# Kernel tuning notes

Measured on AMD Instinct MI355X. Metric: run time of the kernel, lower is better.

Reference implementation:

```python
import jax, jax.numpy as jnp
import numpy as np

N_NODES = 8192
IN_DIM = 128
HIDDEN = 128
N_EDGES = 262144


def gcn_layer(x, W, b, src, dst, n):
    # GCNConv: h = D^{-1/2}(A+I)D^{-1/2} (x @ W) + b, with added self-loops
    h = x @ W  # [n, out]
    loop = jnp.arange(n, dtype=src.dtype)
    s = jnp.concatenate([src, loop])
    d = jnp.concatenate([dst, loop])
    deg = jax.ops.segment_sum(jnp.ones_like(s, dtype=h.dtype), d, num_segments=n)
    dinv = jax.lax.rsqrt(deg)  # deg >= 1 due to self-loops
    norm = dinv[s] * dinv[d]  # [E+n]
    msg = h[s] * norm[:, None]
    out = jax.ops.segment_sum(msg, d, num_segments=n)
    return out + b


def setup_inputs() -> dict:
    key = jax.random.key(0)
    ks = jax.random.split(key, 10)
    g = 1.0 / np.sqrt(HIDDEN)
    inp = {
        "x": jax.random.normal(ks[0], (N_NODES, IN_DIM), dtype=jnp.float32),
        "edge_index": jax.random.randint(ks[1], (2, N_EDGES), 0, N_NODES, dtype=jnp.int32),
        "W1": jax.random.normal(ks[2], (IN_DIM, HIDDEN), dtype=jnp.float32) * (1.0 / np.sqrt(IN_DIM)),
        "b1": jnp.zeros((HIDDEN,), dtype=jnp.float32),
        "W2": jax.random.normal(ks[3], (HIDDEN, HIDDEN), dtype=jnp.float32) * g,
        "b2": jnp.zeros((HIDDEN,), dtype=jnp.float32),
        "W_out": jax.random.normal(ks[4], (HIDDEN, HIDDEN), dtype=jnp.float32) * g,
        "b_out": jnp.zeros((HIDDEN,), dtype=jnp.float32),
        "W_edge": jax.random.normal(ks[5], (2 * HIDDEN,), dtype=jnp.float32) * (1.0 / np.sqrt(2 * HIDDEN)),
        "b_edge": jnp.zeros((), dtype=jnp.float32),
    }
    return inp


def reference(x, edge_index, W1, b1, W2, b2, W_out, b_out, W_edge, b_edge):
    src, dst = edge_index[0], edge_index[1]
    n = x.shape[0]
    h = jax.nn.relu(gcn_layer(x, W1, b1, src, dst, n))
    h = jax.nn.relu(gcn_layer(h, W2, b2, src, dst, n))
    h = h @ W_out + b_out  # [n, hidden]
    # edge_proj(cat(x_i, x_j)) decomposes: logits[i,j] = h_i.w_i + h_j.w_j + b
    w_i, w_j = W_edge[:HIDDEN], W_edge[HIDDEN:]
    a = h @ w_i  # [n]
    c = h @ w_j  # [n]
    edge_logits = a[:, None] + c[None, :] + b_edge  # [n, n]
    return edge_logits
```

## Files before the change

### kernel.cpp

```cpp
#include <hip/hip_runtime.h>

#define NN 8192
#define NE 262144
#define DIM 128
#define BCAP 128

typedef float f32x4 __attribute__((ext_vector_type(4)));
typedef float f32x2 __attribute__((ext_vector_type(2)));

__device__ __forceinline__ float4 f4fma(float s, float4 w, float4 acc) {
    acc.x = fmaf(s, w.x, acc.x);
    acc.y = fmaf(s, w.y, acc.y);
    acc.z = fmaf(s, w.z, acc.z);
    acc.w = fmaf(s, w.w, acc.w);
    return acc;
}
__device__ __forceinline__ float f4dot(float4 a, float4 b) {
    return fmaf(a.x, b.x, fmaf(a.y, b.y, fmaf(a.z, b.z, a.w * b.w)));
}

__global__ __launch_bounds__(256) void zero_kernel(int* __restrict__ cnt) {
    cnt[blockIdx.x * 256 + threadIdx.x] = 0;
}

__global__ __launch_bounds__(256) void fused_pre(const float* __restrict__ X,
                                                 const float* __restrict__ W,
                                                 float* __restrict__ G,
                                                 const int* __restrict__ src,
                                                 const int* __restrict__ dst,
                                                 int* __restrict__ cnt,
                                                 int* __restrict__ bucket,
                                                 const float* __restrict__ Wout,
                                                 const float* __restrict__ bout,
                                                 const float* __restrict__ we,
                                                 const float* __restrict__ bedge,
                                                 float* __restrict__ u,
                                                 float* __restrict__ v,
                                                 float* __restrict__ beta) {
    __shared__ float4 Wl[128 * 32];
    __shared__ float4 Xl[32 * 32];
    int tid = threadIdx.x;
    int bid = blockIdx.x;

    if (bid < 256) {
        int rbase = bid * 32;
        const float4* W4 = (const float4*)W;
#pragma unroll
        for (int i = 0; i < 16; ++i) Wl[i * 256 + tid] = W4[i * 256 + tid];
        const float4* X4 = (const float4*)(X + rbase * DIM);
#pragma unroll
        for (int i = 0; i < 4; ++i) Xl[i * 256 + tid] = X4[i * 256 + tid];
        __syncthreads();

        int tx = tid & 31;
        int ty = tid >> 5;
        float4 acc[4];
#pragma unroll
        for (int i = 0; i < 4; ++i) acc[i] = make_float4(0.f, 0.f, 0.f, 0.f);

        for (int k4 = 0; k4 < 32; ++k4) {
            float4 w0 = Wl[(k4 * 4 + 0) * 32 + tx];
            float4 w1 = Wl[(k4 * 4 + 1) * 32 + tx];
            float4 w2 = Wl[(k4 * 4 + 2) * 32 + tx];
            float4 w3 = Wl[(k4 * 4 + 3) * 32 + tx];
#pragma unroll
            for (int i = 0; i < 4; ++i) {
                float4 xv = Xl[(ty * 4 + i) * 32 + k4];
                acc[i] = f4fma(xv.x, w0, acc[i]);
                acc[i] = f4fma(xv.y, w1, acc[i]);
                acc[i] = f4fma(xv.z, w2, acc[i]);
                acc[i] = f4fma(xv.w, w3, acc[i]);
            }
        }
        float4* G4 = (float4*)G;
#pragma unroll
        for (int i = 0; i < 4; ++i) {
            int r = rbase + ty * 4 + i;
            G4[r * 32 + tx] = acc[i];
        }
        return;
    }
    if (bid < 1280) {
        int e = (bid - 256) * 256 + tid;
        int d = dst[e];
        int p = atomicAdd(&cnt[d], 1);
        if (p < BCAP) bucket[(d << 7) + p] = src[e];
        return;
    }
    float* red = (float*)Xl;
    int k = tid;
    if (k < DIM) {
        const float4* W4o = (const float4*)(Wout + (k << 7));
        const float4* we4 = (const float4*)we;
        float su = 0.f, sv = 0.f;
#pragma unroll
        for (int j = 0; j < 32; ++j) {
            float4 w = W4o[j];
            su += f4dot(w, we4[j]);
            sv += f4dot(w, we4[32 + j]);
        }
        u[k] = su;
        v[k] = sv;
    }
    red[k] = (k < DIM) ? bout[k] * we[k] : 0.f;
    __syncthreads();
    for (int off = 128; off >= 1; off >>= 1) {
        if (k < off) red[k] += red[k + off];
        __syncthreads();
    }
    float b0 = red[0];
    __syncthreads();
    red[k] = (k < DIM) ? bout[k] * we[DIM + k] : 0.f;
    __syncthreads();
    for (int off = 128; off >= 1; off >>= 1) {
        if (k < off) red[k] += red[k + off];
        __syncthreads();
    }
    if (k == 0) {
        beta[0] = b0 + bedge[0];
        beta[1] = red[0];
    }
}

__global__ __launch_bounds__(256) void gather_scale(const float* __restrict__ G1,
                                                    const int* __restrict__ cnt,
                                                    const int* __restrict__ bucket,
                                                    const float* __restrict__ b1,
                                                    float* __restrict__ S2) {
    int node = blockIdx.x * 4 + (threadIdx.x >> 6);
    int lane = threadIdx.x & 63;
    const float2* G12 = (const float2*)G1;

    int degree = cnt[node];
    float dv = rsqrtf((float)(degree + 1));
    int deg = min(degree, BCAP);
    int i0 = bucket[(node << 7) + lane];
    int i1 = bucket[(node << 7) + 64 + lane];

    float2 selfv = G12[node * 64 + lane];
    float ax = selfv.x * dv, ay = selfv.y * dv;
    float px[8], py[8];
#pragma unroll
    for (int k = 0; k < 8; ++k) { px[k] = 0.f; py[k] = 0.f; }

    int d8 = deg & ~7;
    for (int e = 0; e < d8; e += 8) {
        int s[8];
#pragma unroll
        for (int k = 0; k < 8; ++k) s[k] = __shfl((e + k) >= 64 ? i1 : i0, (e + k) & 63);
#pragma unroll
        for (int k = 0; k < 8; ++k) {
            int ck = cnt[s[k]];
            float2 t = G12[s[k] * 64 + lane];
            float w = rsqrtf((float)(ck + 1));
            px[k] = fmaf(t.x, w, px[k]);
            py[k] = fmaf(t.y, w, py[k]);
        }
    }
    for (int e = d8; e < deg; ++e) {
        int s = __shfl(e >= 64 ? i1 : i0, e & 63);
        int ck = cnt[s];
        float2 t = G12[s * 64 + lane];
        float w = rsqrtf((float)(ck + 1));
        ax = fmaf(t.x, w, ax);
        ay = fmaf(t.y, w, ay);
    }
    float yx = ax + ((px[0] + px[1]) + (px[2] + px[3])) + ((px[4] + px[5]) + (px[6] + px[7]));
    float yy = ay + ((py[0] + py[1]) + (py[2] + py[3])) + ((py[4] + py[5]) + (py[6] + py[7]));

    const float2* B2 = (const float2*)b1;
    float2 bb = B2[lane];
    float2 o;
    o.x = fmaxf(fmaf(yx, dv, bb.x), 0.f) * dv;
    o.y = fmaxf(fmaf(yy, dv, bb.y), 0.f) * dv;
    ((float2*)S2)[node * 64 + lane] = o;
}

__global__ __launch_bounds__(256) void gemm_mid(const float* __restrict__ X,
                                                const float* __restrict__ W,
                                                float* __restrict__ G) {
    __shared__ float4 Wl[128 * 32];
    __shared__ float4 Xl[32 * 32];
    int tid = threadIdx.x;
    int rbase = blockIdx.x * 32;

    const float4* W4 = (const float4*)W;
#pragma unroll
    for (int i = 0; i < 16; ++i) Wl[i * 256 + tid] = W4[i * 256 + tid];
    const float4* X4 = (const float4*)(X + rbase * DIM);
#pragma unroll
    for (int i = 0; i < 4; ++i) Xl[i * 256 + tid] = X4[i * 256 + tid];
    __syncthreads();

    int tx = tid & 31;
    int ty = tid >> 5;
    float4 acc[4];
#pragma unroll
    for (int i = 0; i < 4; ++i) acc[i] = make_float4(0.f, 0.f, 0.f, 0.f);

    for (int k4 = 0; k4 < 32; ++k4) {
        float4 w0 = Wl[(k4 * 4 + 0) * 32 + tx];
        float4 w1 = Wl[(k4 * 4 + 1) * 32 + tx];
        float4 w2 = Wl[(k4 * 4 + 2) * 32 + tx];
        float4 w3 = Wl[(k4 * 4 + 3) * 32 + tx];
#pragma unroll
        for (int i = 0; i < 4; ++i) {
            float4 xv = Xl[(ty * 4 + i) * 32 + k4];
            acc[i] = f4fma(xv.x, w0, acc[i]);
            acc[i] = f4fma(xv.y, w1, acc[i]);
            acc[i] = f4fma(xv.z, w2, acc[i]);
            acc[i] = f4fma(xv.w, w3, acc[i]);
        }
    }

    float4* G4 = (float4*)G;
#pragma unroll
    for (int i = 0; i < 4; ++i) {
        int r = rbase + ty * 4 + i;
        G4[r * 32 + tx] = acc[i];
    }
}

__global__ __launch_bounds__(256) void agg_head(const float* __restrict__ G2,
                                                const int* __restrict__ cnt,
                                                const int* __restrict__ bucket,
                                                const float* __restrict__ b2,
                                                const float* __restrict__ u,
                                                const float* __restrict__ v,
                                                const float* __restrict__ beta,
                                                float* __restrict__ a,
                                                float* __restrict__ c) {
    int node = blockIdx.x * 4 + (threadIdx.x >> 6);
    int lane = threadIdx.x & 63;
    const float2* G22 = (const float2*)G2;

    int degree = cnt[node];
    float dv = rsqrtf((float)(degree + 1));
    int deg = min(degree, BCAP);
    int i0 = bucket[(node << 7) + lane];
    int i1 = bucket[(node << 7) + 64 + lane];

    float2 selfv = G22[node * 64 + lane];
    float ax = selfv.x, ay = selfv.y;
    float px[8], py[8];
#pragma unroll
    for (int k = 0; k < 8; ++k) { px[k] = 0.f; py[k] = 0.f; }

    int d8 = deg & ~7;
    for (int e = 0; e < d8; e += 8) {
        int s[8];
#pragma unroll
        for (int k = 0; k < 8; ++k) s[k] = __shfl((e + k) >= 64 ? i1 : i0, (e + k) & 63);
#pragma unroll
        for (int k = 0; k < 8; ++k) {
            float2 t = G22[s[k] * 64 + lane];
            px[k] += t.x;
            py[k] += t.y;
        }
    }
    for (int e = d8; e < deg; ++e) {
        int s = __shfl(e >= 64 ? i1 : i0, e & 63);
        float2 t = G22[s * 64 + lane];
        ax += t.x;
        ay += t.y;
    }
    float yx = ax + ((px[0] + px[1]) + (px[2] + px[3])) + ((px[4] + px[5]) + (px[6] + px[7]));
    float yy = ay + ((py[0] + py[1]) + (py[2] + py[3])) + ((py[4] + py[5]) + (py[6] + py[7]));

    const float2* B2 = (const float2*)b2;
    float2 bb = B2[lane];
    float h0 = fmaxf(fmaf(yx, dv, bb.x), 0.f);
    float h1 = fmaxf(fmaf(yy, dv, bb.y), 0.f);

    float2 uu = ((const float2*)u)[lane];
    float2 vv = ((const float2*)v)[lane];
    float pa = h0 * uu.x + h1 * uu.y;
    float pc = h0 * vv.x + h1 * vv.y;
#pragma unroll
    for (int off = 32; off >= 1; off >>= 1) {
        pa += __shfl_xor(pa, off);
        pc += __shfl_xor(pc, off);
    }
    if (lane == 0) {
        a[node] = pa + beta[0];
        c[node] = pc + beta[1];
    }
}

__global__ __launch_bounds__(256) void out_kernel(const float* __restrict__ a,
                                                  const float* __restrict__ c,
                                                  f32x4* __restrict__ out) {
    const f32x4* c4 = (const f32x4*)c;
    size_t base = (size_t)blockIdx.x * 1024 + threadIdx.x;
#pragma unroll
    for (int q = 0; q < 4; ++q) {
        size_t idx = base + q * 256;
        int i = (int)(idx >> 11);
        int j4 = (int)(idx & 2047);
        f32x4 r = c4[j4] + a[i];
        out[idx] = r;
    }
}

extern "C" void kernel_launch(void* const* d_in, const int* in_sizes, int n_in,
                              void* d_out, int out_size, void* d_ws, size_t ws_size,
                              hipStream_t stream) {
    const float* x    = (const float*)d_in[0];
    const int*   ei   = (const int*)d_in[1];
    const float* W1   = (const float*)d_in[2];
    const float* b1   = (const float*)d_in[3];
    const float* W2   = (const float*)d_in[4];
    const float* b2   = (const float*)d_in[5];
    const float* Wout = (const float*)d_in[6];
    const float* bout = (const float*)d_in[7];
    const float* We   = (const float*)d_in[8];
    const float* bedge= (const float*)d_in[9];
    const int* src = ei;
    const int* dst = ei + NE;

    int* cnt     = (int*)d_ws;
    int* bucket  = cnt + NN;
    float* u     = (float*)(bucket + NN * BCAP);
    float* v     = u + DIM;
    float* beta  = v + DIM;
    float* g1    = beta + 16;
    float* s2    = g1 + NN * DIM;
    float* g2    = s2 + NN * DIM;
    float* av    = g2 + NN * DIM;
    float* cv    = av + NN;

    float* out = (float*)d_out;

    zero_kernel<<<32, 256, 0, stream>>>(cnt);
    fused_pre<<<1281, 256, 0, stream>>>(x, W1, g1, src, dst, cnt, bucket,
                                        Wout, bout, We, bedge, u, v, beta);
    gather_scale<<<NN / 4, 256, 0, stream>>>(g1, cnt, bucket, b1, s2);
    gemm_mid<<<NN / 32, 256, 0, stream>>>(s2, W2, g2);
    agg_head<<<NN / 4, 256, 0, stream>>>(g2, cnt, bucket, b2, u, v, beta, av, cv);
    out_kernel<<<(NN * NN / 4) / 1024, 256, 0, stream>>>(av, cv, (f32x4*)out);
}
```

Before: 109.1 us.

## Split neighbor gathers across half-waves with 16-byte loads and precomputed weights

The two aggregation kernels now give each half of a 64-lane wave a different neighbor, and each lane loads a float4 instead of a float2. The two halves' partial sums are combined with a cross-half shuffle. In gather_scale, each neighbor's degree weight is computed once per lane up front and broadcast by shuffle, instead of being reloaded inside the loop. Padded tail iterations use zero weights instead of a scalar remainder loop, and bucket reads become nontemporal loads. The aim is more memory-level parallelism and fewer load instructions for the random row gathers, at the cost of extra shuffles and some wasted padded loads.

Result: faster. 101.9 us (-6.6%).

```diff
diff --git a/kernel.cpp b/kernel.cpp
--- a/kernel.cpp
+++ b/kernel.cpp
@@ -17,6 +17,13 @@
 }
 __device__ __forceinline__ float f4dot(float4 a, float4 b) {
     return fmaf(a.x, b.x, fmaf(a.y, b.y, fmaf(a.z, b.z, a.w * b.w)));
+}
+__device__ __forceinline__ f32x4 vfma(f32x4 t, float w, f32x4 acc) {
+    acc.x = fmaf(t.x, w, acc.x);
+    acc.y = fmaf(t.y, w, acc.y);
+    acc.z = fmaf(t.z, w, acc.z);
+    acc.w = fmaf(t.w, w, acc.w);
+    return acc;
 }
 
 __global__ __launch_bounds__(256) void zero_kernel(int* __restrict__ cnt) {
@@ -129,51 +136,81 @@
                                                     float* __restrict__ S2) {
     int node = blockIdx.x * 4 + (threadIdx.x >> 6);
     int lane = threadIdx.x & 63;
-    const float2* G12 = (const float2*)G1;
+    int half = lane >> 5;
+    int fl = lane & 31;
+    const f32x4* G14 = (const f32x4*)G1;
 
     int degree = cnt[node];
     float dv = rsqrtf((float)(degree + 1));
     int deg = min(degree, BCAP);
-    int i0 = bucket[(node << 7) + lane];
-    int i1 = bucket[(node << 7) + 64 + lane];
-
-    float2 selfv = G12[node * 64 + lane];
-    float ax = selfv.x * dv, ay = selfv.y * dv;
-    float px[8], py[8];
-#pragma unroll
-    for (int k = 0; k < 8; ++k) { px[k] = 0.f; py[k] = 0.f; }
-
-    int d8 = deg & ~7;
-    for (int e = 0; e < d8; e += 8) {
-        int s[8];
-#pragma unroll
-        for (int k = 0; k < 8; ++k) s[k] = __shfl((e + k) >= 64 ? i1 : i0, (e + k) & 63);
-#pragma unroll
-        for (int k = 0; k < 8; ++k) {
-            int ck = cnt[s[k]];
-            float2 t = G12[s[k] * 64 + lane];
-            float w = rsqrtf((float)(ck + 1));
-            px[k] = fmaf(t.x, w, px[k]);
-            py[k] = fmaf(t.y, w, py[k]);
-        }
-    }
-    for (int e = d8; e < deg; ++e) {
-        int s = __shfl(e >= 64 ? i1 : i0, e & 63);
-        int ck = cnt[s];
-        float2 t = G12[s * 64 + lane];
-        float w = rsqrtf((float)(ck + 1));
-        ax = fmaf(t.x, w, ax);
-        ay = fmaf(t.y, w, ay);
-    }
-    float yx = ax + ((px[0] + px[1]) + (px[2] + px[3])) + ((px[4] + px[5]) + (px[6] + px[7]));
-    float yy = ay + ((py[0] + py[1]) + (py[2] + py[3])) + ((py[4] + py[5]) + (py[6] + py[7]));
-
-    const float2* B2 = (const float2*)b1;
-    float2 bb = B2[lane];
-    float2 o;
-    o.x = fmaxf(fmaf(yx, dv, bb.x), 0.f) * dv;
-    o.y = fmaxf(fmaf(yy, dv, bb.y), 0.f) * dv;
-    ((float2*)S2)[node * 64 + lane] = o;
+    int a0 = __builtin_nontemporal_load(bucket + (node << 7) + lane);
+    int a1 = __builtin_nontemporal_load(bucket + (node << 7) + 64 + lane);
+    int i0s = (lane < deg) ? a0 : 0;
+    int i1s = (64 + lane < deg) ? a1 : 0;
+    float w0 = (lane < deg) ? rsqrtf((float)(cnt[i0s] + 1)) : 0.f;
+    float w1 = (64 + lane < deg) ? rsqrtf((float)(cnt[i1s] + 1)) : 0.f;
+
+    f32x4 zero4 = {0.f, 0.f, 0.f, 0.f};
+    f32x4 p0 = zero4, p1 = zero4, p2 = zero4, p3 = zero4;
+    f32x4 self4 = G14[node * 32 + fl];
+    f32x4 acc = zero4;
+    if (half == 0) {
+        acc.x = self4.x * dv; acc.y = self4.y * dv;
+        acc.z = self4.z * dv; acc.w = self4.w * dv;
+    }
+
+    int L1 = min(deg, 64);
+    int E1 = (L1 + 7) & ~7;
+    for (int e = 0; e < E1; e += 8) {
+        int q = e + half;
+        int s0 = __shfl(i0s, q);     float q0w = __shfl(w0, q);
+        int s1 = __shfl(i0s, q + 2); float q1w = __shfl(w0, q + 2);
+        int s2 = __shfl(i0s, q + 4); float q2w = __shfl(w0, q + 4);
+        int s3 = __shfl(i0s, q + 6); float q3w = __shfl(w0, q + 6);
+        f32x4 t0 = G14[s0 * 32 + fl];
+        f32x4 t1 = G14[s1 * 32 + fl];
+        f32x4 t2 = G14[s2 * 32 + fl];
+        f32x4 t3 = G14[s3 * 32 + fl];
+        p0 = vfma(t0, q0w, p0);
+        p1 = vfma(t1, q1w, p1);
+        p2 = vfma(t2, q2w, p2);
+        p3 = vfma(t3, q3w, p3);
+    }
+    if (deg > 64) {
+        int L2 = deg - 64;
+        int E2 = (L2 + 7) & ~7;
+        for (int e = 0; e < E2; e += 8) {
+            int q = e + half;
+            int s0 = __shfl(i1s, q);     float q0w = __shfl(w1, q);
+            int s1 = __shfl(i1s, q + 2); float q1w = __shfl(w1, q + 2);
+            int s2 = __shfl(i1s, q + 4); float q2w = __shfl(w1, q + 4);
+            int s3 = __shfl(i1s, q + 6); float q3w = __shfl(w1, q + 6);
+            f32x4 t0 = G14[s0 * 32 + fl];
+            f32x4 t1 = G14[s1 * 32 + fl];
+            f32x4 t2 = G14[s2 * 32 + fl];
+            f32x4 t3 = G14[s3 * 32 + fl];
+            p0 = vfma(t0, q0w, p0);
+            p1 = vfma(t1, q1w, p1);
+            p2 = vfma(t2, q2w, p2);
+            p3 = vfma(t3, q3w, p3);
+        }
+    }
+
+    f32x4 sum = ((p0 + p1) + (p2 + p3)) + acc;
+    f32x4 oth;
+    oth.x = __shfl_xor(sum.x, 32);
+    oth.y = __shfl_xor(sum.y, 32);
+    oth.z = __shfl_xor(sum.z, 32);
+    oth.w = __shfl_xor(sum.w, 32);
+    sum += oth;
+
+    f32x4 bb = ((const f32x4*)b1)[fl];
+    f32x4 o;
+    o.x = fmaxf(fmaf(sum.x, dv, bb.x), 0.f) * dv;
+    o.y = fmaxf(fmaf(sum.y, dv, bb.y), 0.f) * dv;
+    o.z = fmaxf(fmaf(sum.z, dv, bb.z), 0.f) * dv;
+    o.w = fmaxf(fmaf(sum.w, dv, bb.w), 0.f) * dv;
+    if (half == 0) ((f32x4*)S2)[node * 32 + fl] = o;
 }
 
 __global__ __launch_bounds__(256) void gemm_mid(const float* __restrict__ X,
@@ -232,52 +269,88 @@
                                                 float* __restrict__ c) {
     int node = blockIdx.x * 4 + (threadIdx.x >> 6);
     int lane = threadIdx.x & 63;
-    const float2* G22 = (const float2*)G2;
+    int half = lane >> 5;
+    int fl = lane & 31;
+    const f32x4* G24 = (const f32x4*)G2;
 
     int degree = cnt[node];
     float dv = rsqrtf((float)(degree + 1));
     int deg = min(degree, BCAP);
-    int i0 = bucket[(node << 7) + lane];
-    int i1 = bucket[(node << 7) + 64 + lane];
-
-    float2 selfv = G22[node * 64 + lane];
-    float ax = selfv.x, ay = selfv.y;
-    float px[8], py[8];
-#pragma unroll
-    for (int k = 0; k < 8; ++k) { px[k] = 0.f; py[k] = 0.f; }
-
-    int d8 = deg & ~7;
-    for (int e = 0; e < d8; e += 8) {
-        int s[8];
-#pragma unroll
-        for (int k = 0; k < 8; ++k) s[k] = __shfl((e + k) >= 64 ? i1 : i0, (e + k) & 63);
-#pragma unroll
-        for (int k = 0; k < 8; ++k) {
-            float2 t = G22[s[k] * 64 + lane];
-            px[k] += t.x;
-            py[k] += t.y;
-        }
-    }
-    for (int e = d8; e < deg; ++e) {
-        int s = __shfl(e >= 64 ? i1 : i0, e & 63);
-        float2 t = G22[s * 64 + lane];
-        ax += t.x;
-        ay += t.y;
-    }
-    float yx = ax + ((px[0] + px[1]) + (px[2] + px[3])) + ((px[4] + px[5]) + (px[6] + px[7]));
-    float yy = ay + ((py[0] + py[1]) + (py[2] + py[3])) + ((py[4] + py[5]) + (py[6] + py[7]));
-
-    const float2* B2 = (const float2*)b2;
-    float2 bb = B2[lane];
-    float h0 = fmaxf(fmaf(yx, dv, bb.x), 0.f);
-    float h1 = fmaxf(fmaf(yy, dv, bb.y), 0.f);
-
-    float2 uu = ((const float2*)u)[lane];
-    float2 vv = ((const float2*)v)[lane];
-    float pa = h0 * uu.x + h1 * uu.y;
-    float pc = h0 * vv.x + h1 * vv.y;
-#pragma unroll
-    for (int off = 32; off >= 1; off >>= 1) {
+    int a0 = __builtin_nontemporal_load(bucket + (node << 7) + lane);
+    int a1 = __builtin_nontemporal_load(bucket + (node << 7) + 64 + lane);
+    int i0s = (lane < deg) ? a0 : 0;
+    int i1s = (64 + lane < deg) ? a1 : 0;
+
+    f32x4 zero4 = {0.f, 0.f, 0.f, 0.f};
+    f32x4 p0 = zero4, p1 = zero4, p2 = zero4, p3 = zero4;
+    f32x4 acc = (half == 0) ? G24[node * 32 + fl] : zero4;
+
+    int L1 = min(deg, 64);
+    int E1 = (L1 + 7) & ~7;
+    for (int e = 0; e < E1; e += 8) {
+        int q = e + half;
+        int s0 = __shfl(i0s, q);
+        int s1 = __shfl(i0s, q + 2);
+        int s2 = __shfl(i0s, q + 4);
+        int s3 = __shfl(i0s, q + 6);
+        float q0w = (q < L1) ? 1.f : 0.f;
+        float q1w = (q + 2 < L1) ? 1.f : 0.f;
+        float q2w = (q + 4 < L1) ? 1.f : 0.f;
+        float q3w = (q + 6 < L1) ? 1.f : 0.f;
+        f32x4 t0 = G24[s0 * 32 + fl];
+        f32x4 t1 = G24[s1 * 32 + fl];
+        f32x4 t2 = G24[s2 * 32 + fl];
+        f32x4 t3 = G24[s3 * 32 + fl];
+        p0 = vfma(t0, q0w, p0);
+        p1 = vfma(t1, q1w, p1);
+        p2 = vfma(t2, q2w, p2);
+        p3 = vfma(t3, q3w, p3);
+    }
+    if (deg > 64) {
+        int L2 = deg - 64;
+        int E2 = (L2 + 7) & ~7;
+        for (int e = 0; e < E2; e += 8) {
+            int q = e + half;
+            int s0 = __shfl(i1s, q);
+            int s1 = __shfl(i1s, q + 2);
+            int s2 = __shfl(i1s, q + 4);
+            int s3 = __shfl(i1s, q + 6);
+            float q0w = (q < L2) ? 1.f : 0.f;
+            float q1w = (q + 2 < L2) ? 1.f : 0.f;
+            float q2w = (q + 4 < L2) ? 1.f : 0.f;
+            float q3w = (q + 6 < L2) ? 1.f : 0.f;
+            f32x4 t0 = G24[s0 * 32 + fl];
+            f32x4 t1 = G24[s1 * 32 + fl];
+            f32x4 t2 = G24[s2 * 32 + fl];
+            f32x4 t3 = G24[s3 * 32 + fl];
+            p0 = vfma(t0, q0w, p0);
+            p1 = vfma(t1, q1w, p1);
+            p2 = vfma(t2, q2w, p2);
+            p3 = vfma(t3, q3w, p3);
+        }
+    }
+
+    f32x4 sum = ((p0 + p1) + (p2 + p3)) + acc;
+    f32x4 oth;
+    oth.x = __shfl_xor(sum.x, 32);
+    oth.y = __shfl_xor(sum.y, 32);
+    oth.z = __shfl_xor(sum.z, 32);
+    oth.w = __shfl_xor(sum.w, 32);
+    sum += oth;
+
+    f32x4 bb = ((const f32x4*)b2)[fl];
+    f32x4 h;
+    h.x = fmaxf(fmaf(sum.x, dv, bb.x), 0.f);
+    h.y = fmaxf(fmaf(sum.y, dv, bb.y), 0.f);
+    h.z = fmaxf(fmaf(sum.z, dv, bb.z), 0.f);
+    h.w = fmaxf(fmaf(sum.w, dv, bb.w), 0.f);
+
+    f32x4 uu = ((const f32x4*)u)[fl];
+    f32x4 vv = ((const f32x4*)v)[fl];
+    float pa = fmaf(h.x, uu.x, fmaf(h.y, uu.y, fmaf(h.z, uu.z, h.w * uu.w)));
+    float pc = fmaf(h.x, vv.x, fmaf(h.y, vv.y, fmaf(h.z, vv.z, h.w * vv.w)));
+#pragma unroll
+    for (int off = 16; off >= 1; off >>= 1) {
         pa += __shfl_xor(pa, off);
         pc += __shfl_xor(pc, off);
     }
```
